# Performance work log

Hardware: AMD Instinct MI355X
Metric: run time of the kernel (lower is better)

## Reference

```python
import jax, jax.numpy as jnp
import numpy as np

B, N, D, NS, H, ITERS = 16, 2048, 128, 8, 128, 3
EPS = 1e-8


def _ln(x, g, b):
    m = jnp.mean(x, -1, keepdims=True)
    v = jnp.mean((x - m) ** 2, -1, keepdims=True)
    return (x - m) * jax.lax.rsqrt(v + 1e-5) * g + b


def _gru(x, h, Wih, Whh, bih, bhh):
    # PyTorch GRUCell math
    gi = x @ Wih.T + bih
    gh = h @ Whh.T + bhh
    ir, iz, inn = jnp.split(gi, 3, -1)
    hr, hz, hn = jnp.split(gh, 3, -1)
    r = jax.nn.sigmoid(ir + hr)
    z = jax.nn.sigmoid(iz + hz)
    n = jnp.tanh(inn + r * hn)
    return (1.0 - z) * n + z * h


def setup_inputs() -> dict:
    key = jax.random.key(0)
    ks = jax.random.split(key, 16)

    def lin(k, out_d, in_d):
        lim = 1.0 / np.sqrt(in_d)
        return jax.random.uniform(k, (out_d, in_d), jnp.float32, -lim, lim)

    return {
        "inputs": jax.random.normal(ks[0], (B, N, D), jnp.float32),
        "init_noise": jax.random.normal(ks[1], (B, NS, 2 * D), jnp.float32),
        "slots_mu": jax.random.normal(ks[2], (1, 1, 2 * D), jnp.float32),
        "slots_logsigma": jax.random.normal(ks[3], (1, 1, 2 * D), jnp.float32) * 0.08,  # ~xavier scale
        "Wq": lin(ks[4], D, D),
        "Wk": lin(ks[5], D, D),
        "gru_Wih": lin(ks[6], 3 * D, D),
        "gru_Whh": lin(ks[7], 3 * D, D),
        "gru_bih": jnp.zeros((3 * D,), jnp.float32),
        "gru_bhh": jnp.zeros((3 * D,), jnp.float32),
        "mlp_mu_W1": lin(ks[8], H, D),
        "mlp_mu_b1": jnp.zeros((H,), jnp.float32),
        "mlp_mu_W2": lin(ks[9], D, H),
        "mlp_mu_b2": jnp.zeros((D,), jnp.float32),
        "ln_in_g": jnp.ones((D,), jnp.float32),
        "ln_in_b": jnp.zeros((D,), jnp.float32),
        "ln_slots_g": jnp.ones((2 * D,), jnp.float32),
        "ln_slots_b": jnp.zeros((2 * D,), jnp.float32),
        "ln_mu_g": jnp.ones((D,), jnp.float32),
        "ln_mu_b": jnp.zeros((D,), jnp.float32),
        "mlp_out_W1": lin(ks[10], 2 * H, 2 * D),
        "mlp_out_b1": jnp.zeros((2 * H,), jnp.float32),
        "mlp_out_W2": lin(ks[11], D, 2 * H),
        "mlp_out_b2": jnp.zeros((D,), jnp.float32),
    }


def _forward(inputs, init_noise, slots_mu, slots_logsigma, Wq, Wk,
             gru_Wih, gru_Whh, gru_bih, gru_bhh,
             mlp_mu_W1, mlp_mu_b1, mlp_mu_W2, mlp_mu_b2,
             ln_in_g, ln_in_b, ln_slots_g, ln_slots_b, ln_mu_g, ln_mu_b,
             mlp_out_W1, mlp_out_b1, mlp_out_W2, mlp_out_b2):
    x = _ln(inputs, ln_in_g, ln_in_b)                      # (B,N,D)
    k = x @ Wk.T
    v = k                                                  # original uses to_k for both k and v
    slots = slots_mu + jnp.exp(slots_logsigma) * init_noise  # (B,NS,2D)
    pi_cl = jnp.full((B, NS, 1), 1.0 / NS, inputs.dtype)

    def step(slots, pi_cl):
        s = _ln(slots, ln_slots_g, ln_slots_b)
        mu_s, ls_s = jnp.split(s, 2, -1)                   # (B,NS,D) each
        q_mu = mu_s @ Wq.T
        q_ls = ls_s @ Wq.T
        inv_var = jnp.exp(-2.0 * q_ls)                     # 1 / exp(q_logsigma)^2
        diff = k[:, None, :, :] - q_mu[:, :, None, :]      # (B,NS,N,D)
        dots = jnp.einsum('bind,bid->bin', diff * diff, inv_var)
        dots_exp = (jnp.exp(-dots) + EPS) * pi_cl          # (B,NS,N)
        gammas = dots_exp / dots_exp.sum(1, keepdims=True)
        attn = gammas / gammas.sum(-1, keepdims=True)
        upd = jnp.einsum('bjd,bij->bid', v, attn)          # (B,NS,D)
        upd = _gru(upd.reshape(-1, D), mu_s.reshape(-1, D),
                   gru_Wih, gru_Whh, gru_bih, gru_bhh).reshape(B, NS, D)
        h = _ln(upd, ln_mu_g, ln_mu_b)
        upd = upd + (jax.nn.relu(h @ mlp_mu_W1.T + mlp_mu_b1) @ mlp_mu_W2.T + mlp_mu_b2)
        diff2 = v[:, None, :, :] - upd[:, :, None, :]      # (B,NS,N,D)
        upd_ls = 0.5 * jnp.log(jnp.einsum('bind,bin->bid', diff2 * diff2 + EPS, attn))
        slots_new = jnp.concatenate([upd, upd_ls], -1)
        pi_new = gammas.sum(-1, keepdims=True)
        pi_new = pi_new / pi_new.shape[2]                  # shape[2]==1: faithful no-op from original
        return slots_new, pi_new

    for _ in range(ITERS):
        slots, pi_cl = step(slots, pi_cl)
    slots, pi_cl = step(jax.lax.stop_gradient(slots), pi_cl)
    h = jax.nn.relu(slots @ mlp_out_W1.T + mlp_out_b1)
    return h @ mlp_out_W2.T + mlp_out_b2                   # (B,NS,D)


def reference(inputs, init_noise, slots_mu, slots_logsigma, Wq, Wk,
              gru_Wih, gru_Whh, gru_bih, gru_bhh,
              mlp_mu_W1, mlp_mu_b1, mlp_mu_W2, mlp_mu_b2,
              ln_in_g, ln_in_b, ln_slots_g, ln_slots_b, ln_mu_g, ln_mu_b,
              mlp_out_W1, mlp_out_b1, mlp_out_W2, mlp_out_b2):
    return _forward(inputs, init_noise, slots_mu, slots_logsigma, Wq, Wk,
                    gru_Wih, gru_Whh, gru_bih, gru_bhh,
                    mlp_mu_W1, mlp_mu_b1, mlp_mu_W2, mlp_mu_b2,
                    ln_in_g, ln_in_b, ln_slots_g, ln_slots_b, ln_mu_g, ln_mu_b,
                    mlp_out_W1, mlp_out_b1, mlp_out_W2, mlp_out_b2)
```

## Files before the change

### kernel.cpp

```cpp
#include <hip/hip_runtime.h>

#define EPS_ 1e-8f

constexpr int OFF_K     = 0;
constexpr int OFF_WQT   = 4194304;
constexpr int OFF_WKT   = OFF_WQT  + 16384;
constexpr int OFF_WIHT  = OFF_WKT  + 16384;
constexpr int OFF_WHHT  = OFF_WIHT + 49152;
constexpr int OFF_WM1T  = OFF_WHHT + 49152;
constexpr int OFF_WM2T  = OFF_WM1T + 16384;
constexpr int OFF_WO1T  = OFF_WM2T + 16384;
constexpr int OFF_WO2T  = OFF_WO1T + 65536;
constexpr int OFF_SLOTS = OFF_WO2T + 32768;
constexpr int OFF_PI    = OFF_SLOTS+ 32768;
constexpr int OFF_MUS   = OFF_PI   + 128;
constexpr int OFF_WA    = OFF_MUS  + 16384;
constexpr int OFF_WB    = OFF_WA   + 16384;
constexpr int OFF_UN    = OFF_WB   + 16384;
constexpr int OFF_S2    = OFF_UN   + 524288;
constexpr int OFF_DEN   = OFF_S2   + 524288;
constexpr int OFF_CZ    = OFF_DEN  + 4096;

__global__ __launch_bounds__(256) void init_kernel(
    const float* __restrict__ Wq,  const float* __restrict__ Wk,
    const float* __restrict__ Wih, const float* __restrict__ Whh,
    const float* __restrict__ Wm1, const float* __restrict__ Wm2,
    const float* __restrict__ Wo1, const float* __restrict__ Wo2,
    const float* __restrict__ smu, const float* __restrict__ sls,
    const float* __restrict__ noise, float* __restrict__ ws) {
  int idx = blockIdx.x * 256 + threadIdx.x;
  if (idx < 16384) { int j = idx >> 7, d = idx & 127; ws[OFF_WQT + d*128 + j] = Wq[idx]; return; }
  idx -= 16384;
  if (idx < 16384) { int j = idx >> 7, d = idx & 127; ws[OFF_WKT + d*128 + j] = Wk[idx]; return; }
  idx -= 16384;
  if (idx < 49152) { int j = idx >> 7, d = idx & 127; ws[OFF_WIHT + d*384 + j] = Wih[idx]; return; }
  idx -= 49152;
  if (idx < 49152) { int j = idx >> 7, d = idx & 127; ws[OFF_WHHT + d*384 + j] = Whh[idx]; return; }
  idx -= 49152;
  if (idx < 16384) { int j = idx >> 7, d = idx & 127; ws[OFF_WM1T + d*128 + j] = Wm1[idx]; return; }
  idx -= 16384;
  if (idx < 16384) { int j = idx >> 7, d = idx & 127; ws[OFF_WM2T + d*128 + j] = Wm2[idx]; return; }
  idx -= 16384;
  if (idx < 65536) { int j = idx >> 8, d = idx & 255; ws[OFF_WO1T + d*256 + j] = Wo1[idx]; return; }
  idx -= 65536;
  if (idx < 32768) { int j = idx >> 8, m = idx & 255; ws[OFF_WO2T + m*128 + j] = Wo2[idx]; return; }
  idx -= 32768;
  if (idx < 32768) { int c = idx & 255; ws[OFF_SLOTS + idx] = smu[c] + expf(sls[c]) * noise[idx]; return; }
  idx -= 32768;
  if (idx < 128) { ws[OFF_PI + idx] = 0.125f; }
}

__global__ __launch_bounds__(256) void k_kernel(
    const float* __restrict__ xin, const float* __restrict__ g, const float* __restrict__ bb,
    const float* __restrict__ WkT, float* __restrict__ kout) {
  __shared__ float xs[64][129];
  __shared__ float2 red2[64][4];
  __shared__ float mrow[64], srow[64];
  int t = threadIdx.x;
  long long base = (long long)blockIdx.x * 64 * 128;
  const float4* in4 = (const float4*)(xin + base);
  for (int f = t; f < 2048; f += 256) {
    float4 v = in4[f];
    int r = f >> 5, c = (f & 31) * 4;
    xs[r][c] = v.x; xs[r][c + 1] = v.y; xs[r][c + 2] = v.z; xs[r][c + 3] = v.w;
  }
  __syncthreads();
  {
    int r = t >> 2, q = t & 3;
    float s = 0.f, ss = 0.f;
    #pragma unroll 8
    for (int u = 0; u < 32; ++u) { float v = xs[r][q * 32 + u]; s += v; ss = fmaf(v, v, ss); }
    red2[r][q] = make_float2(s, ss);
  }
  __syncthreads();
  if (t < 64) {
    float s = 0.f, ss = 0.f;
    #pragma unroll
    for (int q2 = 0; q2 < 4; ++q2) { float2 p = red2[t][q2]; s += p.x; ss += p.y; }
    float m = s * (1.0f / 128.0f);
    float var = ss * (1.0f / 128.0f) - m * m;
    mrow[t] = m; srow[t] = rsqrtf(var + 1e-5f);
  }
  __syncthreads();
  {
    int r = t >> 2, q = t & 3;
    float m = mrow[r], is = srow[r];
    #pragma unroll 8
    for (int u = 0; u < 32; ++u) {
      int d = q * 32 + u;
      xs[r][d] = (xs[r][d] - m) * is * g[d] + bb[d];
    }
  }
  __syncthreads();
  int r = t & 63;
  int jb = __builtin_amdgcn_readfirstlane((t >> 6) * 32);
  float acc[32];
  #pragma unroll
  for (int i = 0; i < 32; ++i) acc[i] = 0.f;
  for (int d = 0; d < 128; ++d) {
    float xv = xs[r][d];
    const float* wrow = WkT + d * 128 + jb;
    #pragma unroll
    for (int i = 0; i < 8; ++i) {
      float4 wv = *(const float4*)(wrow + i * 4);
      acc[i * 4 + 0] = fmaf(xv, wv.x, acc[i * 4 + 0]);
      acc[i * 4 + 1] = fmaf(xv, wv.y, acc[i * 4 + 1]);
      acc[i * 4 + 2] = fmaf(xv, wv.z, acc[i * 4 + 2]);
      acc[i * 4 + 3] = fmaf(xv, wv.w, acc[i * 4 + 3]);
    }
  }
  __syncthreads();
  #pragma unroll 8
  for (int i = 0; i < 32; ++i) xs[r][jb + i] = acc[i];
  __syncthreads();
  float4* out4 = (float4*)(kout + base);
  for (int f = t; f < 2048; f += 256) {
    int rr = f >> 5, c = (f & 31) * 4;
    out4[f] = make_float4(xs[rr][c], xs[rr][c + 1], xs[rr][c + 2], xs[rr][c + 3]);
  }
}

__global__ __launch_bounds__(256) void s1_kernel(
    const float* __restrict__ slots, const float* __restrict__ g, const float* __restrict__ bb,
    const float* __restrict__ WqT, float* __restrict__ mus,
    float* __restrict__ wA, float* __restrict__ wB, float* __restrict__ cz) {
  __shared__ float sl[256];
  __shared__ float2 wr[4];
  __shared__ float qs_l[128], ivs_l[128];
  __shared__ float wrC[4];
  int t = threadIdx.x, bi = blockIdx.x;
  float v = slots[bi * 256 + t];
  float s = v, ss = v * v;
  #pragma unroll
  for (int o = 32; o > 0; o >>= 1) { s += __shfl_down(s, o); ss += __shfl_down(ss, o); }
  if ((t & 63) == 0) wr[t >> 6] = make_float2(s, ss);
  __syncthreads();
  float fs  = wr[0].x + wr[1].x + wr[2].x + wr[3].x;
  float fss = wr[0].y + wr[1].y + wr[2].y + wr[3].y;
  float m   = fs * (1.0f/256.0f);
  float var = fss * (1.0f/256.0f) - m * m;
  float isr = rsqrtf(var + 1e-5f);
  float sn  = (v - m) * isr * g[t] + bb[t];
  sl[t] = sn;
  __syncthreads();
  if (t < 128) {
    float acc = 0.f;
    #pragma unroll 4
    for (int d = 0; d < 128; ++d) acc = fmaf(sl[d], WqT[d * 128 + t], acc);
    qs_l[t] = acc;
    mus[bi * 128 + t] = sn;
  } else {
    int jj = t - 128;
    float acc = 0.f;
    #pragma unroll 4
    for (int d = 0; d < 128; ++d) acc = fmaf(sl[128 + d], WqT[d * 128 + jj], acc);
    ivs_l[jj] = expf(-2.0f * acc);
  }
  __syncthreads();
  float cp = 0.f;
  if (t < 128) {
    float iv = ivs_l[t], q = qs_l[t];
    wA[bi * 128 + t] = iv;
    wB[bi * 128 + t] = -2.0f * q * iv;
    cp = q * q * iv;
  }
  #pragma unroll
  for (int o = 32; o > 0; o >>= 1) cp += __shfl_down(cp, o);
  if ((t & 63) == 0) wrC[t >> 6] = cp;
  __syncthreads();
  if (t == 0) cz[bi] = wrC[0] + wrC[1];
}

__global__ __launch_bounds__(512) void s2_kernel(
    const float* __restrict__ kmat, const float* __restrict__ wA,
    const float* __restrict__ wB,  const float* __restrict__ cz,
    const float* __restrict__ pi,
    float* __restrict__ wun, float* __restrict__ ws2, float* __restrict__ wden) {
  __shared__ float pdots[8][64][8];
  __shared__ float es[64][9];
  __shared__ float recip[64];
  __shared__ float gT[8][72];
  __shared__ float pd[8][8];
  __shared__ float pisl[8], czl[8];
  int t = threadIdx.x;
  int chunk = blockIdx.x, b = blockIdx.y;
  if (t < 8) { pisl[t] = pi[b * 8 + t]; czl[t] = cz[b * 8 + t]; }
  {
    int w = t & 7, n = t >> 3;
    const float4* kr4 = (const float4*)(kmat + (long long)(b * 2048 + chunk * 64 + n) * 128);
    const float4* wa4 = (const float4*)(wA + b * 1024);
    const float4* wb4 = (const float4*)(wB + b * 1024);
    float acc[8] = {0, 0, 0, 0, 0, 0, 0, 0};
    #pragma unroll
    for (int i = 0; i < 4; ++i) {
      int gg = i * 8 + w;
      float4 kv = kr4[gg];
      float xx = kv.x * kv.x, yy = kv.y * kv.y, zz = kv.z * kv.z, ww2 = kv.w * kv.w;
      #pragma unroll
      for (int s = 0; s < 8; ++s) {
        float4 a4 = wa4[s * 32 + gg];
        float4 b4 = wb4[s * 32 + gg];
        float ac = acc[s];
        ac = fmaf(xx, a4.x, ac); ac = fmaf(kv.x, b4.x, ac);
        ac = fmaf(yy, a4.y, ac); ac = fmaf(kv.y, b4.y, ac);
        ac = fmaf(zz, a4.z, ac); ac = fmaf(kv.z, b4.z, ac);
        ac = fmaf(ww2, a4.w, ac); ac = fmaf(kv.w, b4.w, ac);
        acc[s] = ac;
      }
    }
    *(float4*)&pdots[w][n][0] = make_float4(acc[0], acc[1], acc[2], acc[3]);
    *(float4*)&pdots[w][n][4] = make_float4(acc[4], acc[5], acc[6], acc[7]);
  }
  __syncthreads();
  float e;
  {
    int n2 = t >> 3, s = t & 7;
    float dots = czl[s];
    #pragma unroll
    for (int w = 0; w < 8; ++w) dots += pdots[w][n2][s];
    e = (expf(-dots) + EPS_) * pisl[s];
    es[n2][s] = e;
  }
  __syncthreads();
  if (t < 64) {
    float ssum = 0.f;
    #pragma unroll
    for (int s = 0; s < 8; ++s) ssum += es[t][s];
    recip[t] = 1.0f / ssum;
  }
  __syncthreads();
  {
    int n2 = t >> 3, s = t & 7;
    float gam = e * recip[n2];
    gT[s][n2] = gam;
    float p = gam;
    p += __shfl_down(p, 8); p += __shfl_down(p, 16); p += __shfl_down(p, 32);
    if ((t & 63) < 8) pd[t >> 6][t & 7] = p;
  }
  __syncthreads();
  if (t < 8) {
    float sden = 0.f;
    #pragma unroll
    for (int w = 0; w < 8; ++w) sden += pd[w][t];
    wden[(b * 32 + chunk) * 8 + t] = sden;
  }
  {
    int d = t & 127, sh = t >> 7;
    int s0 = sh * 2, s1 = s0 + 1;
    const float* kcol = kmat + (long long)(b * 2048 + chunk * 64) * 128 + d;
    float u0 = 0.f, u1 = 0.f, q0 = 0.f, q1 = 0.f;
    #pragma unroll 2
    for (int n3 = 0; n3 < 64; n3 += 4) {
      float4 ga = *(const float4*)&gT[s0][n3];
      float4 gb = *(const float4*)&gT[s1][n3];
      float k0 = kcol[(n3 + 0) * 128];
      float k1 = kcol[(n3 + 1) * 128];
      float k2 = kcol[(n3 + 2) * 128];
      float k3 = kcol[(n3 + 3) * 128];
      float k0s = k0 * k0, k1s = k1 * k1, k2s = k2 * k2, k3s = k3 * k3;
      u0 = fmaf(ga.x, k0, u0); q0 = fmaf(ga.x, k0s, q0);
      u1 = fmaf(gb.x, k0, u1); q1 = fmaf(gb.x, k0s, q1);
      u0 = fmaf(ga.y, k1, u0); q0 = fmaf(ga.y, k1s, q0);
      u1 = fmaf(gb.y, k1, u1); q1 = fmaf(gb.y, k1s, q1);
      u0 = fmaf(ga.z, k2, u0); q0 = fmaf(ga.z, k2s, q0);
      u1 = fmaf(gb.z, k2, u1); q1 = fmaf(gb.z, k2s, q1);
      u0 = fmaf(ga.w, k3, u0); q0 = fmaf(ga.w, k3s, q0);
      u1 = fmaf(gb.w, k3, u1); q1 = fmaf(gb.w, k3s, q1);
    }
    int pb = ((b * 32 + chunk) * 8) * 128 + d;
    wun[pb + s0 * 128] = u0; wun[pb + s1 * 128] = u1;
    ws2[pb + s0 * 128] = q0; ws2[pb + s1 * 128] = q1;
  }
}

__global__ __launch_bounds__(512) void s3_kernel(
    const float* __restrict__ wun, const float* __restrict__ ws2, const float* __restrict__ wden,
    const float* __restrict__ WihT, const float* __restrict__ WhhT,
    const float* __restrict__ bih,  const float* __restrict__ bhh,
    const float* __restrict__ Wm1T, const float* __restrict__ bm1,
    const float* __restrict__ Wm2T, const float* __restrict__ bm2,
    const float* __restrict__ gmu,  const float* __restrict__ bmu,
    float* __restrict__ slots, float* __restrict__ pi,
    int do_s1,
    const float* __restrict__ gs, const float* __restrict__ bs,
    const float* __restrict__ WqT,
    float* __restrict__ mus, float* __restrict__ wAo, float* __restrict__ wBo,
    float* __restrict__ czo,
    const float* __restrict__ Wo1T, const float* __restrict__ bo1,
    const float* __restrict__ Wo2T, const float* __restrict__ bo2,
    float* __restrict__ out) {
  int t = threadIdx.x, bi = blockIdx.x;
  int d = t & 127, q = t >> 7;
  int b = bi >> 3, i = bi & 7;
  __shared__ float redU[4][128], redS[4][128];
  __shared__ float dred[32];
  __shared__ float xs[128], hs[128];
  __shared__ float gacc[4][6][128];
  __shared__ float ga[6][128];
  __shared__ float grus[128], hl[128], m1s[128];
  __shared__ float macc[4][128];
  __shared__ float2 wr2[2];
  __shared__ float uarr[256];
  float unp = 0.f, s2p = 0.f;
  #pragma unroll
  for (int c = q * 8; c < q * 8 + 8; ++c) {
    int po = ((b * 32 + c) * 8 + i) * 128 + d;
    unp += wun[po]; s2p += ws2[po];
  }
  redU[q][d] = unp; redS[q][d] = s2p;
  if (t < 32) dred[t] = wden[(b * 32 + t) * 8 + i];
  if (q == 1) hs[d] = mus[bi * 128 + d];
  __syncthreads();
  float den = 0.f;
  #pragma unroll
  for (int c = 0; c < 32; ++c) den += dred[c];
  float un  = redU[0][d] + redU[1][d] + redU[2][d] + redU[3][d];
  float s2v = redS[0][d] + redS[1][d] + redS[2][d] + redS[3][d];
  if (q == 0) xs[d] = un / den;
  __syncthreads();
  {
    float a0 = 0, a1 = 0, a2 = 0, a3 = 0, a4 = 0, a5 = 0;
    #pragma unroll 4
    for (int dd = q * 32; dd < q * 32 + 32; ++dd) {
      float xv = xs[dd], hv = hs[dd];
      const float* wi = &WihT[dd * 384 + d];
      const float* wh = &WhhT[dd * 384 + d];
      a0 = fmaf(xv, wi[0],   a0);
      a1 = fmaf(xv, wi[128], a1);
      a2 = fmaf(xv, wi[256], a2);
      a3 = fmaf(hv, wh[0],   a3);
      a4 = fmaf(hv, wh[128], a4);
      a5 = fmaf(hv, wh[256], a5);
    }
    gacc[q][0][d] = a0; gacc[q][1][d] = a1; gacc[q][2][d] = a2;
    gacc[q][3][d] = a3; gacc[q][4][d] = a4; gacc[q][5][d] = a5;
  }
  __syncthreads();
  for (int f = t; f < 768; f += 512) {
    int j = f >> 7, dd = f & 127;
    ga[j][dd] = gacc[0][j][dd] + gacc[1][j][dd] + gacc[2][j][dd] + gacc[3][j][dd];
  }
  __syncthreads();
  float gru = 0.f;
  if (q == 0) {
    float ir = ga[0][d] + bih[d], iz = ga[1][d] + bih[128 + d], inn = ga[2][d] + bih[256 + d];
    float hr = ga[3][d] + bhh[d], hz = ga[4][d] + bhh[128 + d], hn  = ga[5][d] + bhh[256 + d];
    float r  = 1.0f / (1.0f + expf(-(ir + hr)));
    float z  = 1.0f / (1.0f + expf(-(iz + hz)));
    float nn = tanhf(inn + r * hn);
    gru = (1.0f - z) * nn + z * hs[d];
    grus[d] = gru;
    float s = gru, ssq = gru * gru;
    #pragma unroll
    for (int o = 32; o > 0; o >>= 1) { s += __shfl_down(s, o); ssq += __shfl_down(ssq, o); }
    if ((d & 63) == 0) wr2[d >> 6] = make_float2(s, ssq);
  }
  __syncthreads();
  if (q == 0) {
    float fs = wr2[0].x + wr2[1].x, fss = wr2[0].y + wr2[1].y;
    float mean = fs * (1.0f/128.0f);
    float var  = fss * (1.0f/128.0f) - mean * mean;
    hl[d] = (gru - mean) * rsqrtf(var + 1e-5f) * gmu[d] + bmu[d];
  }
  __syncthreads();
  {
    float m1p = 0.f;
    #pragma unroll 4
    for (int dd = q * 32; dd < q * 32 + 32; ++dd)
      m1p = fmaf(hl[dd], Wm1T[dd * 128 + d], m1p);
    macc[q][d] = m1p;
  }
  __syncthreads();
  if (q == 0) m1s[d] = fmaxf(macc[0][d] + macc[1][d] + macc[2][d] + macc[3][d] + bm1[d], 0.f);
  __syncthreads();
  {
    float m2p = 0.f;
    #pragma unroll 4
    for (int dd = q * 32; dd < q * 32 + 32; ++dd)
      m2p = fmaf(m1s[dd], Wm2T[dd * 128 + d], m2p);
    macc[q][d] = m2p;
  }
  __syncthreads();
  if (q == 0) {
    float u = grus[d] + macc[0][d] + macc[1][d] + macc[2][d] + macc[3][d] + bm2[d];
    float val = (s2v - 2.0f * u * un + u * u * den) / den;
    float ls = 0.5f * logf(fmaxf(val, 0.0f) + EPS_);
    slots[bi * 256 + d]       = u;
    slots[bi * 256 + 128 + d] = ls;
    uarr[d] = u; uarr[128 + d] = ls;
    if (d == 0) pi[bi] = den;
  }
  __syncthreads();
  if (do_s1) {
    __shared__ float2 wr4[4];
    __shared__ float sln[256];
    __shared__ float qacc[2][2][128];
    __shared__ float qs_l[128], ivs_l[128];
    __shared__ float wrC[8];
    if (t < 256) {
      float v2 = uarr[t];
      float s = v2, ssq = v2 * v2;
      #pragma unroll
      for (int o = 32; o > 0; o >>= 1) { s += __shfl_down(s, o); ssq += __shfl_down(ssq, o); }
      if ((t & 63) == 0) wr4[t >> 6] = make_float2(s, ssq);
    }
    __syncthreads();
    if (t < 256) {
      float fs  = wr4[0].x + wr4[1].x + wr4[2].x + wr4[3].x;
      float fss = wr4[0].y + wr4[1].y + wr4[2].y + wr4[3].y;
      float m   = fs * (1.0f/256.0f);
      float var = fss * (1.0f/256.0f) - m * m;
      sln[t] = (uarr[t] - m) * rsqrtf(var + 1e-5f) * gs[t] + bs[t];
    }
    __syncthreads();
    {
      int h2 = t >> 8, qq = (t >> 7) & 1, d2 = t & 127;
      const float* src = sln + h2 * 128;
      float acc = 0.f;
      #pragma unroll 4
      for (int dd = qq * 64; dd < qq * 64 + 64; ++dd)
        acc = fmaf(src[dd], WqT[dd * 128 + d2], acc);
      qacc[h2][qq][d2] = acc;
    }
    __syncthreads();
    if (t < 128) {
      qs_l[t] = qacc[0][0][t] + qacc[0][1][t];
      mus[bi * 128 + t] = sln[t];
    } else if (t < 256) {
      int dd2 = t - 128;
      ivs_l[dd2] = expf(-2.0f * (qacc[1][0][dd2] + qacc[1][1][dd2]));
    }
    __syncthreads();
    float cp = 0.f;
    if (t < 128) {
      float iv = ivs_l[t], qv = qs_l[t];
      wAo[bi * 128 + t] = iv;
      wBo[bi * 128 + t] = -2.0f * qv * iv;
      cp = qv * qv * iv;
    }
    #pragma unroll
    for (int o = 32; o > 0; o >>= 1) cp += __shfl_down(cp, o);
    if ((t & 63) == 0) wrC[t >> 6] = cp;
    __syncthreads();
    if (t == 0) czo[bi] = wrC[0] + wrC[1];
  } else {
    __shared__ float oacc[2][256];
    __shared__ float hh[256];
    {
      int o = t & 255, qq = t >> 8;
      float acc = 0.f;
      #pragma unroll 4
      for (int dd = qq * 128; dd < qq * 128 + 128; ++dd)
        acc = fmaf(uarr[dd], Wo1T[dd * 256 + o], acc);
      oacc[qq][o] = acc;
    }
    __syncthreads();
    if (t < 256) hh[t] = fmaxf(oacc[0][t] + oacc[1][t] + bo1[t], 0.f);
    __syncthreads();
    {
      int o2 = t & 127, q4 = t >> 7;
      float acc2 = 0.f;
      #pragma unroll 4
      for (int dd = q4 * 64; dd < q4 * 64 + 64; ++dd)
        acc2 = fmaf(hh[dd], Wo2T[dd * 128 + o2], acc2);
      macc[q4][o2] = acc2;
    }
    __syncthreads();
    if (t < 128) out[bi * 128 + t] = macc[0][t] + macc[1][t] + macc[2][t] + macc[3][t] + bo2[t];
  }
}

extern "C" void kernel_launch(void* const* d_in, const int* in_sizes, int n_in,
                              void* d_out, int out_size, void* d_ws, size_t ws_size,
                              hipStream_t stream) {
  const float* inputs = (const float*)d_in[0];
  const float* noise  = (const float*)d_in[1];
  const float* smu    = (const float*)d_in[2];
  const float* sls    = (const float*)d_in[3];
  const float* Wq     = (const float*)d_in[4];
  const float* Wk     = (const float*)d_in[5];
  const float* Wih    = (const float*)d_in[6];
  const float* Whh    = (const float*)d_in[7];
  const float* bih    = (const float*)d_in[8];
  const float* bhh    = (const float*)d_in[9];
  const float* Wm1    = (const float*)d_in[10];
  const float* bm1    = (const float*)d_in[11];
  const float* Wm2    = (const float*)d_in[12];
  const float* bm2    = (const float*)d_in[13];
  const float* gin    = (const float*)d_in[14];
  const float* bin    = (const float*)d_in[15];
  const float* gsl    = (const float*)d_in[16];
  const float* bsl    = (const float*)d_in[17];
  const float* gmu    = (const float*)d_in[18];
  const float* bmu    = (const float*)d_in[19];
  const float* Wo1    = (const float*)d_in[20];
  const float* bo1    = (const float*)d_in[21];
  const float* Wo2    = (const float*)d_in[22];
  const float* bo2    = (const float*)d_in[23];

  float* ws    = (float*)d_ws;
  float* kbuf  = ws + OFF_K;
  float* WqT   = ws + OFF_WQT;
  float* WkT   = ws + OFF_WKT;
  float* WihT  = ws + OFF_WIHT;
  float* WhhT  = ws + OFF_WHHT;
  float* Wm1T  = ws + OFF_WM1T;
  float* Wm2T  = ws + OFF_WM2T;
  float* Wo1T  = ws + OFF_WO1T;
  float* Wo2T  = ws + OFF_WO2T;
  float* slots = ws + OFF_SLOTS;
  float* pibuf = ws + OFF_PI;
  float* mus   = ws + OFF_MUS;
  float* wA    = ws + OFF_WA;
  float* wB    = ws + OFF_WB;
  float* wun   = ws + OFF_UN;
  float* ws2   = ws + OFF_S2;
  float* wden  = ws + OFF_DEN;
  float* czb   = ws + OFF_CZ;

  hipLaunchKernelGGL(init_kernel, dim3(1153), dim3(256), 0, stream,
                     Wq, Wk, Wih, Whh, Wm1, Wm2, Wo1, Wo2, smu, sls, noise, ws);
  hipLaunchKernelGGL(k_kernel, dim3(512), dim3(256), 0, stream,
                     inputs, gin, bin, WkT, kbuf);
  hipLaunchKernelGGL(s1_kernel, dim3(128), dim3(256), 0, stream,
                     slots, gsl, bsl, WqT, mus, wA, wB, czb);
  for (int s = 0; s < 4; ++s) {
    hipLaunchKernelGGL(s2_kernel, dim3(32, 16), dim3(512), 0, stream,
                       kbuf, wA, wB, czb, pibuf, wun, ws2, wden);
    hipLaunchKernelGGL(s3_kernel, dim3(128), dim3(512), 0, stream,
                       wun, ws2, wden, WihT, WhhT, bih, bhh,
                       Wm1T, bm1, Wm2T, bm2, gmu, bmu, slots, pibuf,
                       (s < 3) ? 1 : 0, gsl, bsl, WqT, mus, wA, wB, czb,
                       Wo1T, bo1, Wo2T, bo2, (float*)d_out);
  }
}
```

Baseline: 185.8 us.

## Retile key projection to 16-row blocks and rebalance s2 dot-product work

The key projection kernel now handles 16 rows per block instead of 64 and launches 2048 blocks. Each thread computes a 2x4 output tile using float4 weight loads and writes directly to global memory, so the shared-memory staging of outputs and the 32-accumulator register array are gone. In s2, each thread now processes two key rows over half the feature dimension, with 16 partial sums per row, which reuses each loaded wA/wB value across two rows. The aim is higher occupancy and less redundant weight traffic, at the cost of a larger shared partial-sum buffer and a longer reduction loop.

Result: faster. 178.2 us (-4.1%).

```diff
diff --git a/kernel.cpp b/kernel.cpp
--- a/kernel.cpp
+++ b/kernel.cpp
@@ -53,71 +53,57 @@
 __global__ __launch_bounds__(256) void k_kernel(
     const float* __restrict__ xin, const float* __restrict__ g, const float* __restrict__ bb,
     const float* __restrict__ WkT, float* __restrict__ kout) {
-  __shared__ float xs[64][129];
-  __shared__ float2 red2[64][4];
-  __shared__ float mrow[64], srow[64];
+  __shared__ float xs[16][129];
+  __shared__ float2 red[16][16];
+  __shared__ float mrow[16], srow[16];
   int t = threadIdx.x;
-  long long base = (long long)blockIdx.x * 64 * 128;
+  long long base = (long long)blockIdx.x * 16 * 128;
   const float4* in4 = (const float4*)(xin + base);
-  for (int f = t; f < 2048; f += 256) {
+  for (int f = t; f < 512; f += 256) {
     float4 v = in4[f];
     int r = f >> 5, c = (f & 31) * 4;
     xs[r][c] = v.x; xs[r][c + 1] = v.y; xs[r][c + 2] = v.z; xs[r][c + 3] = v.w;
   }
   __syncthreads();
   {
-    int r = t >> 2, q = t & 3;
+    int row = t >> 4, l = t & 15;
     float s = 0.f, ss = 0.f;
-    #pragma unroll 8
-    for (int u = 0; u < 32; ++u) { float v = xs[r][q * 32 + u]; s += v; ss = fmaf(v, v, ss); }
-    red2[r][q] = make_float2(s, ss);
-  }
-  __syncthreads();
-  if (t < 64) {
+    #pragma unroll
+    for (int dd = 0; dd < 128; dd += 16) { float v = xs[row][dd + l]; s += v; ss = fmaf(v, v, ss); }
+    red[row][l] = make_float2(s, ss);
+  }
+  __syncthreads();
+  if (t < 16) {
     float s = 0.f, ss = 0.f;
     #pragma unroll
-    for (int q2 = 0; q2 < 4; ++q2) { float2 p = red2[t][q2]; s += p.x; ss += p.y; }
+    for (int l = 0; l < 16; ++l) { float2 p = red[t][l]; s += p.x; ss += p.y; }
     float m = s * (1.0f / 128.0f);
     float var = ss * (1.0f / 128.0f) - m * m;
-    mrow[t] = m; srow[t] = rsqrtf(var + 1e-5f);
-  }
-  __syncthreads();
-  {
-    int r = t >> 2, q = t & 3;
-    float m = mrow[r], is = srow[r];
-    #pragma unroll 8
-    for (int u = 0; u < 32; ++u) {
-      int d = q * 32 + u;
-      xs[r][d] = (xs[r][d] - m) * is * g[d] + bb[d];
-    }
-  }
-  __syncthreads();
-  int r = t & 63;
-  int jb = __builtin_amdgcn_readfirstlane((t >> 6) * 32);
-  float acc[32];
-  #pragma unroll
-  for (int i = 0; i < 32; ++i) acc[i] = 0.f;
+    mrow[t] = m;
+    srow[t] = rsqrtf(var + 1e-5f);
+  }
+  __syncthreads();
+  for (int f = t; f < 2048; f += 256) {
+    int row = f >> 7, d = f & 127;
+    xs[row][d] = (xs[row][d] - mrow[row]) * srow[row] * g[d] + bb[d];
+  }
+  __syncthreads();
+  int j4 = t & 31, rg = t >> 5;
+  int r0 = rg * 2;
+  float a00 = 0, a01 = 0, a02 = 0, a03 = 0;
+  float a10 = 0, a11 = 0, a12 = 0, a13 = 0;
+  #pragma unroll 4
   for (int d = 0; d < 128; ++d) {
-    float xv = xs[r][d];
-    const float* wrow = WkT + d * 128 + jb;
-    #pragma unroll
-    for (int i = 0; i < 8; ++i) {
-      float4 wv = *(const float4*)(wrow + i * 4);
-      acc[i * 4 + 0] = fmaf(xv, wv.x, acc[i * 4 + 0]);
-      acc[i * 4 + 1] = fmaf(xv, wv.y, acc[i * 4 + 1]);
-      acc[i * 4 + 2] = fmaf(xv, wv.z, acc[i * 4 + 2]);
-      acc[i * 4 + 3] = fmaf(xv, wv.w, acc[i * 4 + 3]);
-    }
-  }
-  __syncthreads();
-  #pragma unroll 8
-  for (int i = 0; i < 32; ++i) xs[r][jb + i] = acc[i];
-  __syncthreads();
-  float4* out4 = (float4*)(kout + base);
-  for (int f = t; f < 2048; f += 256) {
-    int rr = f >> 5, c = (f & 31) * 4;
-    out4[f] = make_float4(xs[rr][c], xs[rr][c + 1], xs[rr][c + 2], xs[rr][c + 3]);
-  }
+    float4 wv = *(const float4*)(WkT + d * 128 + j4 * 4);
+    float x0 = xs[r0][d], x1 = xs[r0 + 1][d];
+    a00 = fmaf(x0, wv.x, a00); a01 = fmaf(x0, wv.y, a01);
+    a02 = fmaf(x0, wv.z, a02); a03 = fmaf(x0, wv.w, a03);
+    a10 = fmaf(x1, wv.x, a10); a11 = fmaf(x1, wv.y, a11);
+    a12 = fmaf(x1, wv.z, a12); a13 = fmaf(x1, wv.w, a13);
+  }
+  float* o0 = kout + base + (long long)r0 * 128 + j4 * 4;
+  *(float4*)o0         = make_float4(a00, a01, a02, a03);
+  *(float4*)(o0 + 128) = make_float4(a10, a11, a12, a13);
 }
 
 __global__ __launch_bounds__(256) void s1_kernel(
@@ -176,7 +162,7 @@
     const float* __restrict__ wB,  const float* __restrict__ cz,
     const float* __restrict__ pi,
     float* __restrict__ wun, float* __restrict__ ws2, float* __restrict__ wden) {
-  __shared__ float pdots[8][64][8];
+  __shared__ float pdots[16][64][8];
   __shared__ float es[64][9];
   __shared__ float recip[64];
   __shared__ float gT[8][72];
@@ -186,30 +172,40 @@
   int chunk = blockIdx.x, b = blockIdx.y;
   if (t < 8) { pisl[t] = pi[b * 8 + t]; czl[t] = cz[b * 8 + t]; }
   {
-    int w = t & 7, n = t >> 3;
-    const float4* kr4 = (const float4*)(kmat + (long long)(b * 2048 + chunk * 64 + n) * 128);
+    int w = t & 15, nt = t >> 4;
+    int n0 = nt * 2;
+    const float4* kr4 = (const float4*)(kmat + (long long)(b * 2048 + chunk * 64) * 128);
     const float4* wa4 = (const float4*)(wA + b * 1024);
     const float4* wb4 = (const float4*)(wB + b * 1024);
-    float acc[8] = {0, 0, 0, 0, 0, 0, 0, 0};
-    #pragma unroll
-    for (int i = 0; i < 4; ++i) {
-      int gg = i * 8 + w;
-      float4 kv = kr4[gg];
-      float xx = kv.x * kv.x, yy = kv.y * kv.y, zz = kv.z * kv.z, ww2 = kv.w * kv.w;
+    float acc0[8] = {0,0,0,0,0,0,0,0};
+    float acc1[8] = {0,0,0,0,0,0,0,0};
+    #pragma unroll
+    for (int i = 0; i < 2; ++i) {
+      int gg = i * 16 + w;
+      float4 k0 = kr4[n0 * 32 + gg];
+      float4 k1 = kr4[(n0 + 1) * 32 + gg];
+      float x0 = k0.x * k0.x, y0 = k0.y * k0.y, z0 = k0.z * k0.z, w0 = k0.w * k0.w;
+      float x1 = k1.x * k1.x, y1 = k1.y * k1.y, z1 = k1.z * k1.z, w1 = k1.w * k1.w;
       #pragma unroll
       for (int s = 0; s < 8; ++s) {
         float4 a4 = wa4[s * 32 + gg];
         float4 b4 = wb4[s * 32 + gg];
-        float ac = acc[s];
-        ac = fmaf(xx, a4.x, ac); ac = fmaf(kv.x, b4.x, ac);
-        ac = fmaf(yy, a4.y, ac); ac = fmaf(kv.y, b4.y, ac);
-        ac = fmaf(zz, a4.z, ac); ac = fmaf(kv.z, b4.z, ac);
-        ac = fmaf(ww2, a4.w, ac); ac = fmaf(kv.w, b4.w, ac);
-        acc[s] = ac;
+        float c0 = acc0[s], c1 = acc1[s];
+        c0 = fmaf(x0, a4.x, c0); c0 = fmaf(k0.x, b4.x, c0);
+        c0 = fmaf(y0, a4.y, c0); c0 = fmaf(k0.y, b4.y, c0);
+        c0 = fmaf(z0, a4.z, c0); c0 = fmaf(k0.z, b4.z, c0);
+        c0 = fmaf(w0, a4.w, c0); c0 = fmaf(k0.w, b4.w, c0);
+        c1 = fmaf(x1, a4.x, c1); c1 = fmaf(k1.x, b4.x, c1);
+        c1 = fmaf(y1, a4.y, c1); c1 = fmaf(k1.y, b4.y, c1);
+        c1 = fmaf(z1, a4.z, c1); c1 = fmaf(k1.z, b4.z, c1);
+        c1 = fmaf(w1, a4.w, c1); c1 = fmaf(k1.w, b4.w, c1);
+        acc0[s] = c0; acc1[s] = c1;
       }
     }
-    *(float4*)&pdots[w][n][0] = make_float4(acc[0], acc[1], acc[2], acc[3]);
-    *(float4*)&pdots[w][n][4] = make_float4(acc[4], acc[5], acc[6], acc[7]);
+    *(float4*)&pdots[w][n0][0]     = make_float4(acc0[0], acc0[1], acc0[2], acc0[3]);
+    *(float4*)&pdots[w][n0][4]     = make_float4(acc0[4], acc0[5], acc0[6], acc0[7]);
+    *(float4*)&pdots[w][n0 + 1][0] = make_float4(acc1[0], acc1[1], acc1[2], acc1[3]);
+    *(float4*)&pdots[w][n0 + 1][4] = make_float4(acc1[4], acc1[5], acc1[6], acc1[7]);
   }
   __syncthreads();
   float e;
@@ -217,7 +213,7 @@
     int n2 = t >> 3, s = t & 7;
     float dots = czl[s];
     #pragma unroll
-    for (int w = 0; w < 8; ++w) dots += pdots[w][n2][s];
+    for (int w = 0; w < 16; ++w) dots += pdots[w][n2][s];
     e = (expf(-dots) + EPS_) * pisl[s];
     es[n2][s] = e;
   }
@@ -520,7 +516,7 @@
 
   hipLaunchKernelGGL(init_kernel, dim3(1153), dim3(256), 0, stream,
                      Wq, Wk, Wih, Whh, Wm1, Wm2, Wo1, Wo2, smu, sls, noise, ws);
-  hipLaunchKernelGGL(k_kernel, dim3(512), dim3(256), 0, stream,
+  hipLaunchKernelGGL(k_kernel, dim3(2048), dim3(256), 0, stream,
                      inputs, gin, bin, WkT, kbuf);
   hipLaunchKernelGGL(s1_kernel, dim3(128), dim3(256), 0, stream,
                      slots, gsl, bsl, WqT, mus, wA, wB, czb);
```
